# Optimization experiments

Measured on AMD Instinct MI355X. Metric: run time of the kernel, lower is better.

Reference implementation:

```python
import jax, jax.numpy as jnp
import numpy as np
from itertools import product

B, C, HH, WW, DD, N = 2, 32, 96, 96, 96, 30000


def setup_inputs() -> dict:
    key = jax.random.key(0)
    k1, k2, k3 = jax.random.split(key, 3)
    voxel_features = jax.random.normal(k1, (B, C, HH, WW, DD), dtype=jnp.float32)
    # vertices in normalized [-1, 1] grid_sample coordinates (x, y, z)
    vertices = jax.random.uniform(k2, (B, N, 3), dtype=jnp.float32, minval=-1.0, maxval=1.0)
    fan_in = C * 27
    conv_w = jax.random.normal(k3, (C, C, 1, 27), dtype=jnp.float32) * np.sqrt(2.0 / fan_in)
    conv_b = jnp.zeros((C,), dtype=jnp.float32)
    return {
        "voxel_features": voxel_features,
        "vertices": vertices,
        "conv_w": conv_w,
        "conv_b": conv_b,
        "img_H": HH,
        "img_W": WW,
        "img_D": DD,
    }


def _trilinear_sample(voxel_features, grid):
    """grid_sample(mode='bilinear', padding_mode='border', align_corners=True).
    voxel_features: (B,C,H,W,D); grid: (B,N,K,3) with (x,y,z) in [-1,1],
    x -> D axis, y -> W axis, z -> H axis. Returns (B,C,N,K)."""
    b, c, h, w, d = voxel_features.shape
    x, y, z = grid[..., 0], grid[..., 1], grid[..., 2]
    ix = jnp.clip((x + 1.0) * 0.5 * (d - 1), 0.0, d - 1)
    iy = jnp.clip((y + 1.0) * 0.5 * (w - 1), 0.0, w - 1)
    iz = jnp.clip((z + 1.0) * 0.5 * (h - 1), 0.0, h - 1)
    x0 = jnp.floor(ix).astype(jnp.int32); x1 = jnp.minimum(x0 + 1, d - 1)
    y0 = jnp.floor(iy).astype(jnp.int32); y1 = jnp.minimum(y0 + 1, w - 1)
    z0 = jnp.floor(iz).astype(jnp.int32); z1 = jnp.minimum(z0 + 1, h - 1)
    fx = ix - x0; fy = iy - y0; fz = iz - z0
    vf = voxel_features.reshape(b, c, h * w * d)
    n, k = grid.shape[1], grid.shape[2]

    def gather(zi, yi, xi):
        lin = (zi * w + yi) * d + xi  # (B,N,K)
        g = jnp.take_along_axis(vf, lin.reshape(b, 1, n * k), axis=2)
        return g.reshape(b, c, n, k)

    def wgt(wz, wy, wx):
        return (wz * wy * wx)[:, None]  # (B,1,N,K)

    out = (
        gather(z0, y0, x0) * wgt(1 - fz, 1 - fy, 1 - fx)
        + gather(z0, y0, x1) * wgt(1 - fz, 1 - fy, fx)
        + gather(z0, y1, x0) * wgt(1 - fz, fy, 1 - fx)
        + gather(z0, y1, x1) * wgt(1 - fz, fy, fx)
        + gather(z1, y0, x0) * wgt(fz, 1 - fy, 1 - fx)
        + gather(z1, y0, x1) * wgt(fz, 1 - fy, fx)
        + gather(z1, y1, x0) * wgt(fz, fy, 1 - fx)
        + gather(z1, y1, x1) * wgt(fz, fy, fx)
    )
    return out


def reference(voxel_features, vertices, conv_w, conv_b, img_H, img_W, img_D):
    # 27 neighbor offsets in normalized coords, scaled per (x,y,z) component
    offs = jnp.asarray(list(product((-1, 0, 1), repeat=3)), dtype=jnp.float32)  # (27,3)
    scale = jnp.array(
        [2.0 / (img_D - 1), 2.0 / (img_W - 1), 2.0 / (img_H - 1)], dtype=jnp.float32
    )
    shift = offs * scale  # (27,3)
    grid = vertices[:, :, None, :] + shift[None, None]  # (B,N,27,3)
    feats = _trilinear_sample(voxel_features, grid)  # (B,C,N,27)
    # Conv2d(C,C,(1,27)): weighted reduction over (C_in, 27) -> (B,N,C_out)
    out = jnp.einsum("bink,oik->bno", feats, conv_w[:, :, 0, :]) + conv_b
    return out
```

## Files before the change

### kernel.cpp

```cpp
#include <hip/hip_runtime.h>
#include <stdint.h>

#define HWD 884736ull
#define NV 30000
#define AST 1032

typedef __attribute__((ext_vector_type(8))) __bf16 bf16x8;
typedef __attribute__((ext_vector_type(4))) float f32x4;
typedef __attribute__((ext_vector_type(4))) unsigned int uint4v;

__device__ __forceinline__ unsigned short f2bf(float f) {
    union { float f; unsigned int u; } v; v.f = f;
    unsigned int u = v.u;
    return (unsigned short)((u + 0x7FFFu + ((u >> 16) & 1u)) >> 16);
}

__device__ __forceinline__ float bf2f(unsigned short s) {
    union { unsigned int u; float f; } v;
    v.u = ((unsigned int)s) << 16;
    return v.f;
}

__device__ __forceinline__ void axis_setup(float coord, float sc, int& wstart, float w[3][4]) {
    int i0[3], i1[3];
    float fr[3];
#pragma unroll
    for (int a = 0; a < 3; ++a) {
        float g = coord + (float)(a - 1) * sc;
        float ix = (g + 1.0f) * 0.5f * 95.0f;
        ix = fminf(fmaxf(ix, 0.0f), 95.0f);
        float fl = floorf(ix);
        int x0 = (int)fl;
        i0[a] = x0;
        i1[a] = min(x0 + 1, 95);
        fr[a] = ix - fl;
    }
    int ws = min(max(i0[1] - 1, 0), 92);
    wstart = ws;
#pragma unroll
    for (int a = 0; a < 3; ++a) {
        int d0 = min(max(i0[a] - ws, 0), 3);
        int d1 = min(max(i1[a] - ws, 0), 3);
        float f1 = fr[a], f0 = 1.0f - f1;
#pragma unroll
        for (int j = 0; j < 4; ++j)
            w[a][j] = (d0 == j ? f0 : 0.0f) + (d1 == j ? f1 : 0.0f);
    }
}

__global__ __launch_bounds__(256) void prep_kernel(const float* __restrict__ cw,
                                                   unsigned short* __restrict__ Wp) {
    int gid = blockIdx.x * 256 + threadIdx.x;
    int j = gid & 7;
    int l = (gid >> 3) & 63;
    int t = (gid >> 9) & 1;
    int s = gid >> 10;
    int kk = ((l >> 4) & 3) * 8 + j;
    int o = t * 16 + (l & 15);
    float v = 0.0f;
    if (kk < 27) v = cw[(size_t)o * 864 + s * 27 + kk];
    Wp[gid] = f2bf(v);
}

__global__ __launch_bounds__(256) void transpose_kernel(const float* __restrict__ vox,
                                                        unsigned short* __restrict__ voxT) {
    int blk = blockIdx.x;
    int tid = threadIdx.x;
    int b = blk / 9216;
    int zy = blk % 9216;
    const float* src = vox + (size_t)b * 32 * HWD + (size_t)zy * 96;
    unsigned short* dst = voxT + (size_t)blk * 3072;
#pragma unroll
    for (int i = 0; i < 3; ++i) {
        int idx = i * 256 + tid;
        int c = idx & 31;
        int x4 = idx >> 5;
        f32x4 v = *(const f32x4*)(src + (size_t)c * HWD + x4 * 4);
#pragma unroll
        for (int k = 0; k < 4; ++k)
            dst[(x4 * 4 + k) * 32 + c] = f2bf(v[k]);
    }
}

__global__ __launch_bounds__(512) void fused_kernel(const unsigned short* __restrict__ voxT,
                                                    const float* __restrict__ verts,
                                                    const unsigned short* __restrict__ Wp,
                                                    const float* __restrict__ bias,
                                                    float* __restrict__ out) {
    __shared__ unsigned short At[16 * AST];
    int tid = threadIdx.x;
    int vl = tid >> 5;
    int c = tid & 31;
    int vg = (int)blockIdx.x * 16 + vl;

    const float* vp = verts + (size_t)vg * 3;
    float vx = vp[0], vy = vp[1], vz = vp[2];
    const float sc = 2.0f / 95.0f;
    int wsx, wsy, wsz;
    float wx[3][4], wy[3][4], wz[3][4];
    axis_setup(vx, sc, wsx, wx);
    axis_setup(vy, sc, wsy, wy);
    axis_setup(vz, sc, wsz, wz);
    int bb = (vg >= NV) ? 1 : 0;
    const unsigned short* vb = voxT + (size_t)bb * HWD * 32 + c;

    float f[27];
#pragma unroll
    for (int k = 0; k < 27; ++k) f[k] = 0.0f;

#pragma unroll
    for (int tz = 0; tz < 4; ++tz) {
        float rx[4][3];
#pragma unroll
        for (int ty = 0; ty < 4; ++ty) {
            const unsigned short* row =
                vb + (((size_t)(wsz + tz) * 96 + (size_t)(wsy + ty)) * 96 + wsx) * 32;
            float b0 = bf2f(row[0]);
            float b1 = bf2f(row[32]);
            float b2 = bf2f(row[64]);
            float b3 = bf2f(row[96]);
#pragma unroll
            for (int a = 0; a < 3; ++a)
                rx[ty][a] = b0 * wx[a][0] + b1 * wx[a][1] + b2 * wx[a][2] + b3 * wx[a][3];
        }
        float ry[3][3];
#pragma unroll
        for (int b = 0; b < 3; ++b)
#pragma unroll
            for (int a = 0; a < 3; ++a)
                ry[b][a] = rx[0][a] * wy[b][0] + rx[1][a] * wy[b][1] +
                           rx[2][a] * wy[b][2] + rx[3][a] * wy[b][3];
#pragma unroll
        for (int g = 0; g < 3; ++g)
#pragma unroll
            for (int b = 0; b < 3; ++b)
#pragma unroll
                for (int a = 0; a < 3; ++a)
                    f[9 * a + 3 * b + g] += wz[g][tz] * ry[b][a];
    }

    unsigned int pk[16];
#pragma unroll
    for (int i = 0; i < 16; ++i) {
        float lo = (2 * i < 27) ? f[2 * i] : 0.0f;
        float hi = (2 * i + 1 < 27) ? f[2 * i + 1] : 0.0f;
        pk[i] = (unsigned int)f2bf(lo) | ((unsigned int)f2bf(hi) << 16);
    }
    uint4v* dst = (uint4v*)&At[vl * AST + c * 32];
    uint4v s0 = {pk[0], pk[1], pk[2], pk[3]};
    uint4v s1 = {pk[4], pk[5], pk[6], pk[7]};
    uint4v s2 = {pk[8], pk[9], pk[10], pk[11]};
    uint4v s3 = {pk[12], pk[13], pk[14], pk[15]};
    dst[0] = s0; dst[1] = s1; dst[2] = s2; dst[3] = s3;

    __syncthreads();

    int wv = tid >> 6;
    if (wv < 2) {
        int lane = tid & 63;
        int mrow = lane & 15, quad = lane >> 4;
        const bf16x8* wp = (const bf16x8*)Wp;
        const unsigned short* arow = &At[mrow * AST + quad * 8];
        f32x4 acc = {0.f, 0.f, 0.f, 0.f};
#pragma unroll 8
        for (int s = 0; s < 32; ++s) {
            bf16x8 a = *(const bf16x8*)(arow + s * 32);
            bf16x8 b = wp[(s * 2 + wv) * 64 + lane];
            acc = __builtin_amdgcn_mfma_f32_16x16x32_bf16(a, b, acc, 0, 0, 0);
        }
        float bs = bias[wv * 16 + mrow];
#pragma unroll
        for (int r = 0; r < 4; ++r) {
            int v = (int)blockIdx.x * 16 + quad * 4 + r;
            out[(size_t)v * 32 + wv * 16 + mrow] = acc[r] + bs;
        }
    }
}

extern "C" void kernel_launch(void* const* d_in, const int* in_sizes, int n_in,
                              void* d_out, int out_size, void* d_ws, size_t ws_size,
                              hipStream_t stream) {
    const float* vox = (const float*)d_in[0];
    const float* verts = (const float*)d_in[1];
    const float* cw = (const float*)d_in[2];
    const float* cb = (const float*)d_in[3];
    float* out = (float*)d_out;

    unsigned short* Wp = (unsigned short*)d_ws;
    unsigned short* voxT = (unsigned short*)((char*)d_ws + 65536);

    hipLaunchKernelGGL(prep_kernel, dim3(128), dim3(256), 0, stream, cw, Wp);
    hipLaunchKernelGGL(transpose_kernel, dim3(18432), dim3(256), 0, stream, vox, voxT);
    hipLaunchKernelGGL(fused_kernel, dim3(3750), dim3(512), 0, stream,
                       voxT, verts, Wp, cb, out);
}
```

Baseline: 418.1 us.

## Process two channels per thread with packed loads and swizzled LDS stores

Each thread now handles a channel pair, loading 32-bit words holding two bf16 values instead of single shorts, which halves the threads per block (256) and duplicates the per-vertex axis setup less often. The separable interpolation is restructured to fold the y-axis weights into the x loop with fewer temporaries. The LDS staging layout is changed to an XOR-swizzled chunk order to avoid bank conflicts on the wide stores, with matching index math in the MFMA read loop. Register pressure rises from holding 54 accumulators per thread, which may limit occupancy.

```diff
diff --git a/kernel.cpp b/kernel.cpp
--- a/kernel.cpp
+++ b/kernel.cpp
@@ -7,6 +7,7 @@
 
 typedef __attribute__((ext_vector_type(8))) __bf16 bf16x8;
 typedef __attribute__((ext_vector_type(4))) float f32x4;
+typedef __attribute__((ext_vector_type(2))) float f32x2;
 typedef __attribute__((ext_vector_type(4))) unsigned int uint4v;
 
 __device__ __forceinline__ unsigned short f2bf(float f) {
@@ -15,10 +16,18 @@
     return (unsigned short)((u + 0x7FFFu + ((u >> 16) & 1u)) >> 16);
 }
 
-__device__ __forceinline__ float bf2f(unsigned short s) {
-    union { unsigned int u; float f; } v;
-    v.u = ((unsigned int)s) << 16;
-    return v.f;
+__device__ __forceinline__ f32x2 up2(unsigned int u) {
+    union { unsigned int u; float f; } lo, hi;
+    lo.u = u << 16;
+    hi.u = u & 0xffff0000u;
+    f32x2 r = {lo.f, hi.f};
+    return r;
+}
+
+__device__ __forceinline__ f32x2 fma2s(f32x2 x, float s, f32x2 acc) {
+    acc[0] = fmaf(x[0], s, acc[0]);
+    acc[1] = fmaf(x[1], s, acc[1]);
+    return acc;
 }
 
 __device__ __forceinline__ void axis_setup(float coord, float sc, int& wstart, float w[3][4]) {
@@ -82,15 +91,16 @@
     }
 }
 
-__global__ __launch_bounds__(512) void fused_kernel(const unsigned short* __restrict__ voxT,
-                                                    const float* __restrict__ verts,
-                                                    const unsigned short* __restrict__ Wp,
-                                                    const float* __restrict__ bias,
-                                                    float* __restrict__ out) {
-    __shared__ unsigned short At[16 * AST];
+__global__ __launch_bounds__(256, 4) void fused_kernel(const unsigned short* __restrict__ voxT,
+                                                       const float* __restrict__ verts,
+                                                       const unsigned short* __restrict__ Wp,
+                                                       const float* __restrict__ bias,
+                                                       float* __restrict__ out) {
+    __shared__ __align__(16) unsigned short At[16 * AST];
     int tid = threadIdx.x;
-    int vl = tid >> 5;
-    int c = tid & 31;
+    int vl = tid >> 4;
+    int cp = tid & 15;
+    int c0 = cp * 2;
     int vg = (int)blockIdx.x * 16 + vl;
 
     const float* vp = verts + (size_t)vg * 3;
@@ -102,56 +112,61 @@
     axis_setup(vy, sc, wsy, wy);
     axis_setup(vz, sc, wsz, wz);
     int bb = (vg >= NV) ? 1 : 0;
-    const unsigned short* vb = voxT + (size_t)bb * HWD * 32 + c;
-
-    float f[27];
-#pragma unroll
-    for (int k = 0; k < 27; ++k) f[k] = 0.0f;
+    const unsigned short* vb = voxT + (size_t)bb * HWD * 32 + c0;
+
+    f32x2 f2[27];
+#pragma unroll
+    for (int k = 0; k < 27; ++k) f2[k] = (f32x2){0.0f, 0.0f};
 
 #pragma unroll
     for (int tz = 0; tz < 4; ++tz) {
-        float rx[4][3];
+        f32x2 ry[9];
+#pragma unroll
+        for (int i = 0; i < 9; ++i) ry[i] = (f32x2){0.0f, 0.0f};
 #pragma unroll
         for (int ty = 0; ty < 4; ++ty) {
-            const unsigned short* row =
-                vb + (((size_t)(wsz + tz) * 96 + (size_t)(wsy + ty)) * 96 + wsx) * 32;
-            float b0 = bf2f(row[0]);
-            float b1 = bf2f(row[32]);
-            float b2 = bf2f(row[64]);
-            float b3 = bf2f(row[96]);
-#pragma unroll
-            for (int a = 0; a < 3; ++a)
-                rx[ty][a] = b0 * wx[a][0] + b1 * wx[a][1] + b2 * wx[a][2] + b3 * wx[a][3];
-        }
-        float ry[3][3];
-#pragma unroll
-        for (int b = 0; b < 3; ++b)
-#pragma unroll
-            for (int a = 0; a < 3; ++a)
-                ry[b][a] = rx[0][a] * wy[b][0] + rx[1][a] * wy[b][1] +
-                           rx[2][a] * wy[b][2] + rx[3][a] * wy[b][3];
+            const unsigned int* row = (const unsigned int*)(
+                vb + (((size_t)(wsz + tz) * 96 + (size_t)(wsy + ty)) * 96 + wsx) * 32);
+            unsigned int u0 = row[0], u1 = row[16], u2 = row[32], u3 = row[48];
+            f32x2 b0 = up2(u0), b1 = up2(u1), b2 = up2(u2), b3 = up2(u3);
+#pragma unroll
+            for (int a = 0; a < 3; ++a) {
+                f32x2 rxt = (f32x2){0.0f, 0.0f};
+                rxt = fma2s(b0, wx[a][0], rxt);
+                rxt = fma2s(b1, wx[a][1], rxt);
+                rxt = fma2s(b2, wx[a][2], rxt);
+                rxt = fma2s(b3, wx[a][3], rxt);
+#pragma unroll
+                for (int b = 0; b < 3; ++b)
+                    ry[3 * b + a] = fma2s(rxt, wy[b][ty], ry[3 * b + a]);
+            }
+        }
 #pragma unroll
         for (int g = 0; g < 3; ++g)
 #pragma unroll
             for (int b = 0; b < 3; ++b)
 #pragma unroll
                 for (int a = 0; a < 3; ++a)
-                    f[9 * a + 3 * b + g] += wz[g][tz] * ry[b][a];
-    }
-
-    unsigned int pk[16];
-#pragma unroll
-    for (int i = 0; i < 16; ++i) {
-        float lo = (2 * i < 27) ? f[2 * i] : 0.0f;
-        float hi = (2 * i + 1 < 27) ? f[2 * i + 1] : 0.0f;
-        pk[i] = (unsigned int)f2bf(lo) | ((unsigned int)f2bf(hi) << 16);
-    }
-    uint4v* dst = (uint4v*)&At[vl * AST + c * 32];
-    uint4v s0 = {pk[0], pk[1], pk[2], pk[3]};
-    uint4v s1 = {pk[4], pk[5], pk[6], pk[7]};
-    uint4v s2 = {pk[8], pk[9], pk[10], pk[11]};
-    uint4v s3 = {pk[12], pk[13], pk[14], pk[15]};
-    dst[0] = s0; dst[1] = s1; dst[2] = s2; dst[3] = s3;
+                    f2[9 * a + 3 * b + g] = fma2s(ry[3 * b + a], wz[g][tz], f2[9 * a + 3 * b + g]);
+    }
+
+    unsigned short* basep = &At[vl * AST + cp * 64];
+    int rot = cp & 7;
+#pragma unroll
+    for (int j = 0; j < 8; ++j) {
+        const int ch = j >> 2;
+        const int kb = (j & 3) * 8;
+        unsigned int pw[4];
+#pragma unroll
+        for (int t2 = 0; t2 < 4; ++t2) {
+            int k0 = kb + 2 * t2, k1 = k0 + 1;
+            float lo = (k0 < 27) ? f2[k0][ch] : 0.0f;
+            float hi = (k1 < 27) ? f2[k1][ch] : 0.0f;
+            pw[t2] = (unsigned int)f2bf(lo) | ((unsigned int)f2bf(hi) << 16);
+        }
+        uint4v s = {pw[0], pw[1], pw[2], pw[3]};
+        *(uint4v*)(basep + (j ^ rot) * 8) = s;
+    }
 
     __syncthreads();
 
@@ -160,11 +175,12 @@
         int lane = tid & 63;
         int mrow = lane & 15, quad = lane >> 4;
         const bf16x8* wp = (const bf16x8*)Wp;
-        const unsigned short* arow = &At[mrow * AST + quad * 8];
         f32x4 acc = {0.f, 0.f, 0.f, 0.f};
 #pragma unroll 8
         for (int s = 0; s < 32; ++s) {
-            bf16x8 a = *(const bf16x8*)(arow + s * 32);
+            int u = s * 4 + quad;
+            int p = u ^ ((u >> 3) & 7);
+            bf16x8 a = *(const bf16x8*)&At[mrow * AST + p * 8];
             bf16x8 b = wp[(s * 2 + wv) * 64 + lane];
             acc = __builtin_amdgcn_mfma_f32_16x16x32_bf16(a, b, acc, 0, 0, 0);
         }
@@ -191,6 +207,6 @@
 
     hipLaunchKernelGGL(prep_kernel, dim3(128), dim3(256), 0, stream, cw, Wp);
     hipLaunchKernelGGL(transpose_kernel, dim3(18432), dim3(256), 0, stream, vox, voxT);
-    hipLaunchKernelGGL(fused_kernel, dim3(3750), dim3(512), 0, stream,
+    hipLaunchKernelGGL(fused_kernel, dim3(3750), dim3(256), 0, stream,
                        voxT, verts, Wp, cb, out);
 }
```

Result: slower. 920.9 us (+120.3%).

## Pack voxels in x-quads per channel and swizzle shared-memory A tile

Applied to the files above, without the earlier changes.

The transposed voxel layout now groups four consecutive x values of one channel into an 8-byte word. Each gather row therefore takes two 8-byte loads instead of four 2-byte loads, with the x weights shifted into a 7-tap window by the quad offset. The shared-memory A tile now uses an XOR-style rotation of its 16-byte chunks to reduce LDS bank conflicts on the stores and on the MFMA operand reads. The y/z accumulation is restructured into fused FMAs, at the cost of more weight arithmetic per row.

```diff
diff --git a/kernel.cpp b/kernel.cpp
--- a/kernel.cpp
+++ b/kernel.cpp
@@ -7,6 +7,7 @@
 
 typedef __attribute__((ext_vector_type(8))) __bf16 bf16x8;
 typedef __attribute__((ext_vector_type(4))) float f32x4;
+typedef __attribute__((ext_vector_type(2))) unsigned int uint2v;
 typedef __attribute__((ext_vector_type(4))) unsigned int uint4v;
 
 __device__ __forceinline__ unsigned short f2bf(float f) {
@@ -15,10 +16,11 @@
     return (unsigned short)((u + 0x7FFFu + ((u >> 16) & 1u)) >> 16);
 }
 
-__device__ __forceinline__ float bf2f(unsigned short s) {
-    union { unsigned int u; float f; } v;
-    v.u = ((unsigned int)s) << 16;
-    return v.f;
+__device__ __forceinline__ float bf_lo(unsigned int u) {
+    union { unsigned int u; float f; } v; v.u = u << 16; return v.f;
+}
+__device__ __forceinline__ float bf_hi(unsigned int u) {
+    union { unsigned int u; float f; } v; v.u = u & 0xffff0000u; return v.f;
 }
 
 __device__ __forceinline__ void axis_setup(float coord, float sc, int& wstart, float w[3][4]) {
@@ -63,31 +65,32 @@
 }
 
 __global__ __launch_bounds__(256) void transpose_kernel(const float* __restrict__ vox,
-                                                        unsigned short* __restrict__ voxT) {
+                                                        uint2v* __restrict__ voxQ) {
     int blk = blockIdx.x;
     int tid = threadIdx.x;
     int b = blk / 9216;
     int zy = blk % 9216;
     const float* src = vox + (size_t)b * 32 * HWD + (size_t)zy * 96;
-    unsigned short* dst = voxT + (size_t)blk * 3072;
+    uint2v* dst = voxQ + (size_t)blk * 768;
 #pragma unroll
     for (int i = 0; i < 3; ++i) {
         int idx = i * 256 + tid;
         int c = idx & 31;
-        int x4 = idx >> 5;
-        f32x4 v = *(const f32x4*)(src + (size_t)c * HWD + x4 * 4);
-#pragma unroll
-        for (int k = 0; k < 4; ++k)
-            dst[(x4 * 4 + k) * 32 + c] = f2bf(v[k]);
-    }
-}
-
-__global__ __launch_bounds__(512) void fused_kernel(const unsigned short* __restrict__ voxT,
+        int q = idx >> 5;
+        f32x4 v = *(const f32x4*)(src + (size_t)c * HWD + q * 4);
+        unsigned int u0 = (unsigned int)f2bf(v[0]) | ((unsigned int)f2bf(v[1]) << 16);
+        unsigned int u1 = (unsigned int)f2bf(v[2]) | ((unsigned int)f2bf(v[3]) << 16);
+        uint2v p = {u0, u1};
+        dst[q * 32 + c] = p;
+    }
+}
+
+__global__ __launch_bounds__(512) void fused_kernel(const uint2v* __restrict__ voxQ,
                                                     const float* __restrict__ verts,
                                                     const unsigned short* __restrict__ Wp,
                                                     const float* __restrict__ bias,
                                                     float* __restrict__ out) {
-    __shared__ unsigned short At[16 * AST];
+    __shared__ __align__(16) unsigned short At[16 * AST];
     int tid = threadIdx.x;
     int vl = tid >> 5;
     int c = tid & 31;
@@ -101,8 +104,30 @@
     axis_setup(vx, sc, wsx, wx);
     axis_setup(vy, sc, wsy, wy);
     axis_setup(vz, sc, wsz, wz);
+
+    int o = wsx & 3;
+    bool s1 = (o & 1) != 0, s2 = (o & 2) != 0;
+    float wx7[3][7];
+#pragma unroll
+    for (int a = 0; a < 3; ++a) {
+        float t0 = s1 ? 0.0f : wx[a][0];
+        float t1 = s1 ? wx[a][0] : wx[a][1];
+        float t2 = s1 ? wx[a][1] : wx[a][2];
+        float t3 = s1 ? wx[a][2] : wx[a][3];
+        float t4 = s1 ? wx[a][3] : 0.0f;
+        wx7[a][0] = s2 ? 0.0f : t0;
+        wx7[a][1] = s2 ? 0.0f : t1;
+        wx7[a][2] = s2 ? t0 : t2;
+        wx7[a][3] = s2 ? t1 : t3;
+        wx7[a][4] = s2 ? t2 : t4;
+        wx7[a][5] = s2 ? t3 : 0.0f;
+        wx7[a][6] = s2 ? t4 : 0.0f;
+    }
+    int q0 = wsx >> 2;
+    int q1 = min(q0 + 1, 23);
+
     int bb = (vg >= NV) ? 1 : 0;
-    const unsigned short* vb = voxT + (size_t)bb * HWD * 32 + c;
+    const uint2v* Qb = voxQ + (size_t)bb * 9216 * 768 + c;
 
     float f[27];
 #pragma unroll
@@ -110,48 +135,51 @@
 
 #pragma unroll
     for (int tz = 0; tz < 4; ++tz) {
-        float rx[4][3];
+        float ry[9];
+#pragma unroll
+        for (int i = 0; i < 9; ++i) ry[i] = 0.0f;
 #pragma unroll
         for (int ty = 0; ty < 4; ++ty) {
-            const unsigned short* row =
-                vb + (((size_t)(wsz + tz) * 96 + (size_t)(wsy + ty)) * 96 + wsx) * 32;
-            float b0 = bf2f(row[0]);
-            float b1 = bf2f(row[32]);
-            float b2 = bf2f(row[64]);
-            float b3 = bf2f(row[96]);
-#pragma unroll
-            for (int a = 0; a < 3; ++a)
-                rx[ty][a] = b0 * wx[a][0] + b1 * wx[a][1] + b2 * wx[a][2] + b3 * wx[a][3];
-        }
-        float ry[3][3];
-#pragma unroll
-        for (int b = 0; b < 3; ++b)
-#pragma unroll
-            for (int a = 0; a < 3; ++a)
-                ry[b][a] = rx[0][a] * wy[b][0] + rx[1][a] * wy[b][1] +
-                           rx[2][a] * wy[b][2] + rx[3][a] * wy[b][3];
+            size_t r = ((size_t)(wsz + tz) * 96 + (size_t)(wsy + ty)) * 24;
+            uint2v A = Qb[(r + q0) * 32];
+            uint2v Bq = Qb[(r + q1) * 32];
+            float b0 = bf_lo(A[0]), b1 = bf_hi(A[0]), b2 = bf_lo(A[1]), b3 = bf_hi(A[1]);
+            float b4 = bf_lo(Bq[0]), b5 = bf_hi(Bq[0]), b6 = bf_lo(Bq[1]);
+#pragma unroll
+            for (int a = 0; a < 3; ++a) {
+                float rxt = b0 * wx7[a][0] + b1 * wx7[a][1] + b2 * wx7[a][2] +
+                            b3 * wx7[a][3] + b4 * wx7[a][4] + b5 * wx7[a][5] +
+                            b6 * wx7[a][6];
+#pragma unroll
+                for (int b = 0; b < 3; ++b)
+                    ry[3 * b + a] = fmaf(rxt, wy[b][ty], ry[3 * b + a]);
+            }
+        }
 #pragma unroll
         for (int g = 0; g < 3; ++g)
 #pragma unroll
             for (int b = 0; b < 3; ++b)
 #pragma unroll
                 for (int a = 0; a < 3; ++a)
-                    f[9 * a + 3 * b + g] += wz[g][tz] * ry[b][a];
-    }
-
-    unsigned int pk[16];
-#pragma unroll
-    for (int i = 0; i < 16; ++i) {
-        float lo = (2 * i < 27) ? f[2 * i] : 0.0f;
-        float hi = (2 * i + 1 < 27) ? f[2 * i + 1] : 0.0f;
-        pk[i] = (unsigned int)f2bf(lo) | ((unsigned int)f2bf(hi) << 16);
-    }
-    uint4v* dst = (uint4v*)&At[vl * AST + c * 32];
-    uint4v s0 = {pk[0], pk[1], pk[2], pk[3]};
-    uint4v s1 = {pk[4], pk[5], pk[6], pk[7]};
-    uint4v s2 = {pk[8], pk[9], pk[10], pk[11]};
-    uint4v s3 = {pk[12], pk[13], pk[14], pk[15]};
-    dst[0] = s0; dst[1] = s1; dst[2] = s2; dst[3] = s3;
+                    f[9 * a + 3 * b + g] = fmaf(ry[3 * b + a], wz[g][tz], f[9 * a + 3 * b + g]);
+    }
+
+    unsigned short* rowp = &At[vl * AST];
+#pragma unroll
+    for (int j = 0; j < 4; ++j) {
+        const int kb = j * 8;
+        unsigned int pw[4];
+#pragma unroll
+        for (int t2 = 0; t2 < 4; ++t2) {
+            int k0 = kb + 2 * t2, k1 = k0 + 1;
+            float lo = (k0 < 27) ? f[k0] : 0.0f;
+            float hi = (k1 < 27) ? f[k1] : 0.0f;
+            pw[t2] = (unsigned int)f2bf(lo) | ((unsigned int)f2bf(hi) << 16);
+        }
+        uint4v s = {pw[0], pw[1], pw[2], pw[3]};
+        int p = c * 4 + ((j + c) & 3);
+        *(uint4v*)(rowp + p * 8) = s;
+    }
 
     __syncthreads();
 
@@ -160,11 +188,11 @@
         int lane = tid & 63;
         int mrow = lane & 15, quad = lane >> 4;
         const bf16x8* wp = (const bf16x8*)Wp;
-        const unsigned short* arow = &At[mrow * AST + quad * 8];
         f32x4 acc = {0.f, 0.f, 0.f, 0.f};
 #pragma unroll 8
         for (int s = 0; s < 32; ++s) {
-            bf16x8 a = *(const bf16x8*)(arow + s * 32);
+            int p = s * 4 + ((quad + s) & 3);
+            bf16x8 a = *(const bf16x8*)&At[mrow * AST + p * 8];
             bf16x8 b = wp[(s * 2 + wv) * 64 + lane];
             acc = __builtin_amdgcn_mfma_f32_16x16x32_bf16(a, b, acc, 0, 0, 0);
         }
@@ -187,10 +215,10 @@
     float* out = (float*)d_out;
 
     unsigned short* Wp = (unsigned short*)d_ws;
-    unsigned short* voxT = (unsigned short*)((char*)d_ws + 65536);
+    uint2v* voxQ = (uint2v*)((char*)d_ws + 65536);
 
     hipLaunchKernelGGL(prep_kernel, dim3(128), dim3(256), 0, stream, cw, Wp);
-    hipLaunchKernelGGL(transpose_kernel, dim3(18432), dim3(256), 0, stream, vox, voxT);
+    hipLaunchKernelGGL(transpose_kernel, dim3(18432), dim3(256), 0, stream, vox, voxQ);
     hipLaunchKernelGGL(fused_kernel, dim3(3750), dim3(512), 0, stream,
-                       voxT, verts, Wp, cb, out);
-}
+                       voxQ, verts, Wp, cb, out);
+}
```

Result: slower. 457.1 us (+9.3%).
